# Kernel optimization log

Hardware: AMD Instinct MI355X
Metric: run time of the kernel (lower is better)

The kernel has to match this reference:

```python
import jax, jax.numpy as jnp
import numpy as np

B, T, DIM = 4, 1024, 1024
HEADS, DH = 16, 64
MEM, CMEM, RATIO = 1024, 256, 4
KV = CMEM + MEM + T  # 2304
TOTAL_MEM = MEM + CMEM  # 1280
NEG = -np.finfo(np.float32).max


def shift(x):
    # Faithful port of the pad/flatten/reshape relative-position shift trick.
    b, h, i, j = x.shape
    x = jnp.concatenate([x, jnp.zeros((b, h, i, i), x.dtype)], axis=-1)  # [b,h,i,i+j]
    l = i + j - 1
    x = x.reshape(b, h, i * (i + j))
    pad = (-x.shape[-1]) % l
    x = jnp.pad(x, ((0, 0), (0, 0), (0, pad)))
    x = x.reshape(b, h, -1, l)
    return x[:, :, :i, i - 1:]  # [b,h,i,j]


def setup_inputs() -> dict:
    key = jax.random.key(0)
    ks = jax.random.split(key, 10)
    s = 0.02
    return {
        "x": jax.random.normal(ks[0], (B, T, DIM), jnp.float32),
        "mem": jax.random.normal(ks[1], (B, MEM, DIM), jnp.float32),
        "cmem": jax.random.normal(ks[2], (B, CMEM, DIM), jnp.float32),
        "pos_emb": jax.random.normal(ks[3], (HEADS, KV, DH), jnp.float32),
        "input_mask": jnp.ones((B, T), bool),
        "Wq": jax.random.normal(ks[4], (DIM, DIM), jnp.float32) * s,
        "Wkv": jax.random.normal(ks[5], (2 * DIM, DIM), jnp.float32) * s,
        "Wout": jax.random.normal(ks[6], (DIM, DIM), jnp.float32) * s,
        "bout": jnp.zeros((DIM,), jnp.float32),
        "conv_w": jax.random.normal(ks[7], (DIM, DIM, RATIO), jnp.float32) * s,
        "conv_b": jnp.zeros((DIM,), jnp.float32),
    }


def reference(x, mem, cmem, pos_emb, input_mask, Wq, Wkv, Wout, bout, conv_w, conv_b):
    b, t, e = x.shape
    scale = DH ** -0.5

    q = x @ Wq.T                                             # [b,t,e]
    kv_input = jnp.concatenate([cmem, mem, x], axis=1)       # [b,kv,e]
    kv_len = kv_input.shape[1]
    kv = kv_input @ Wkv.T                                    # [b,kv,2e]
    k, v = jnp.split(kv, 2, axis=-1)

    def mh(z):
        return z.reshape(z.shape[0], z.shape[1], HEADS, DH).transpose(0, 2, 1, 3)

    qh, kh, vh = mh(q), mh(k), mh(v)                         # [b,h,*,dh]

    dots = jnp.einsum('bhid,bhjd->bhij', qh, kh) * scale     # [b,h,t,kv]

    pe = pos_emb[:, -kv_len:].astype(qh.dtype)               # [h,kv,dh]
    pos_dots = shift(jnp.einsum('bhid,hjd->bhij', qh, pe) * scale)
    dots = dots + pos_dots

    # input mask (padded True over mem+cmem positions)
    m = input_mask[:, None, :, None] & input_mask[:, None, None, :]  # [b,1,t,t]
    m = jnp.pad(m, ((0, 0), (0, 0), (0, 0), (TOTAL_MEM, 0)), constant_values=True)
    dots = jnp.where(m, dots, NEG)

    # causal mask shifted by total memory length
    causal = jnp.triu(jnp.ones((t, t + TOTAL_MEM), bool), k=1 + TOTAL_MEM)
    dots = jnp.where(causal[None, None], NEG, dots)

    attn = jax.nn.softmax(dots, axis=-1)
    out = jnp.einsum('bhij,bhjd->bhid', attn, vh)
    out = out.transpose(0, 2, 1, 3).reshape(b, t, e)
    logits = out @ Wout.T + bout

    # memory update (eval path, calc_memory=True)
    queue = jnp.concatenate([mem, x], axis=1)                # [b,mem+t,e]
    new_mem = queue[:, -MEM:]
    old_mem = jax.lax.stop_gradient(queue[:, :-MEM])         # [b,t,e], t % RATIO == 0
    comp = jax.lax.conv_general_dilated(
        old_mem.transpose(0, 2, 1), conv_w, (RATIO,), 'VALID',
        dimension_numbers=('NCH', 'OIH', 'NCH')) + conv_b[None, :, None]
    comp = comp.transpose(0, 2, 1)                           # [b,t//RATIO,e]
    new_cmem = jnp.concatenate([cmem, comp], axis=1)[:, -CMEM:]

    return logits, new_mem, new_cmem
```

## Files before the change

kernel.cpp:

```cpp
#include <hip/hip_runtime.h>
#include <hip/hip_bf16.h>
#include <hip/hip_fp16.h>
#include <cstdint>
#include <cstddef>
#include <cstring>

using bf16 = __hip_bfloat16;

constexpr int TS    = 1024;
constexpr int DIM   = 1024;
constexpr int MEMN  = 1024;
constexpr int CMEMN = 256;
constexpr int KVN   = 2304;
constexpr int TMEM  = 1280;

typedef __attribute__((ext_vector_type(8))) short short8;
typedef __attribute__((ext_vector_type(4))) float f32x4;

__device__ __forceinline__ unsigned short f2bf_us(float f){
    __hip_bfloat16 t = __float2bfloat16(f);
    unsigned short us; memcpy(&us, &t, 2); return us;
}
__device__ __forceinline__ int sw8(int row){ return (row & 7) ^ ((row >> 3) & 7); }

__device__ __forceinline__ short8 ldfrag(const unsigned short* base, int row, int chunk) {
    int ch = chunk ^ sw8(row);
    return *(const short8*)(base + row*64 + ch*8);
}
__device__ __forceinline__ void gl2lds16(const void* g, void* l) {
    __builtin_amdgcn_global_load_lds(
        (const __attribute__((address_space(1))) void*)g,
        (__attribute__((address_space(3))) void*)l, 16, 0, 0);
}

__global__ __launch_bounds__(256) void pack(
    const float* __restrict__ x, const float* __restrict__ memp,
    const float* __restrict__ cmem, const float* __restrict__ Wq,
    const float* __restrict__ Wkv, const float* __restrict__ Wout,
    const float* __restrict__ cw, const float* __restrict__ pe,
    unsigned short* __restrict__ kvin, unsigned short* __restrict__ wqb,
    unsigned short* __restrict__ wkvb, unsigned short* __restrict__ woutb,
    unsigned short* __restrict__ cw2b, unsigned short* __restrict__ peb)
{
    const size_t t8 = ((size_t)blockIdx.x * 256 + threadIdx.x) * 8;
    unsigned short h[8];
    if (t8 < 9437184) {
        size_t g = t8 >> 10;
        int cc = (int)(t8 & 1023);
        int b = (int)(g / KVN), j = (int)(g % KVN);
        const float* src;
        if (j < CMEMN)      src = cmem + ((size_t)b*CMEMN + j)*1024 + cc;
        else if (j < TMEM)  src = memp + ((size_t)b*MEMN + (j - CMEMN))*1024 + cc;
        else                src = x    + ((size_t)b*TS   + (j - TMEM))*1024 + cc;
        float4 f0 = *(const float4*)src; float4 f1 = *(const float4*)(src + 4);
        h[0]=f2bf_us(f0.x); h[1]=f2bf_us(f0.y); h[2]=f2bf_us(f0.z); h[3]=f2bf_us(f0.w);
        h[4]=f2bf_us(f1.x); h[5]=f2bf_us(f1.y); h[6]=f2bf_us(f1.z); h[7]=f2bf_us(f1.w);
        *(uint4*)(kvin + t8) = *(const uint4*)h;
    } else if (t8 < 13631488) {
        const float* src; unsigned short* dst; float sc = 1.0f;
        if (t8 < 10485760)      { src = Wq   + (t8 - 9437184);  dst = wqb   + (t8 - 9437184); sc = 0.125f; }
        else if (t8 < 12582912) { src = Wkv  + (t8 - 10485760); dst = wkvb  + (t8 - 10485760); }
        else                    { src = Wout + (t8 - 12582912); dst = woutb + (t8 - 12582912); }
        float4 f0 = *(const float4*)src; float4 f1 = *(const float4*)(src + 4);
        h[0]=f2bf_us(f0.x*sc); h[1]=f2bf_us(f0.y*sc); h[2]=f2bf_us(f0.z*sc); h[3]=f2bf_us(f0.w*sc);
        h[4]=f2bf_us(f1.x*sc); h[5]=f2bf_us(f1.y*sc); h[6]=f2bf_us(f1.z*sc); h[7]=f2bf_us(f1.w*sc);
        *(uint4*)dst = *(const uint4*)h;
    } else if (t8 < 17825792) {
        size_t o8 = t8 - 13631488;
        int o = (int)(o8 >> 12); int rem = (int)(o8 & 4095);
        int r = rem >> 10, i = rem & 1023;
        #pragma unroll
        for (int p = 0; p < 8; ++p) h[p] = f2bf_us(cw[(o << 12) + (i + p)*4 + r]);
        *(uint4*)(cw2b + o8) = *(const uint4*)h;
    } else {
        size_t o8 = t8 - 17825792;
        const float* src = pe + o8;
        float4 f0 = *(const float4*)src; float4 f1 = *(const float4*)(src + 4);
        h[0]=f2bf_us(f0.x); h[1]=f2bf_us(f0.y); h[2]=f2bf_us(f0.z); h[3]=f2bf_us(f0.w);
        h[4]=f2bf_us(f1.x); h[5]=f2bf_us(f1.y); h[6]=f2bf_us(f1.z); h[7]=f2bf_us(f1.w);
        *(uint4*)(peb + o8) = *(const uint4*)h;
    }
}

template<int EPI, int QMODE>
__global__ __launch_bounds__(256) void gemm_mfma(
    const bf16* __restrict__ Abf, const bf16* __restrict__ Bbf,
    const float* __restrict__ bias, void* __restrict__ Cptr,
    void* __restrict__ C2, int M, int N, int K)
{
    __shared__ alignas(16) unsigned short As[128*64];
    __shared__ alignas(16) unsigned short Bs[128*64];
    const int tid = threadIdx.x, lane = tid & 63, w = tid >> 6;
    const int quad = lane >> 4, colq = lane & 15;
    const int wm = w >> 1, wn = w & 1;
    const int m0 = blockIdx.x * 128, n0 = blockIdx.y * 128;
    size_t abase;
    if (QMODE == 0)      abase = (size_t)m0 * K;
    else if (QMODE == 1) abase = ((size_t)((m0 >> 10)*KVN + TMEM + (m0 & 1023))) * 1024;
    else                 abase = ((size_t)((m0 >> 8)*KVN + CMEMN)) * 1024 + (size_t)(m0 & 255) * 4096;
    const unsigned short* Ag = (const unsigned short*)Abf + abase;
    const unsigned short* Bg = (const unsigned short*)Bbf + (size_t)n0 * K;

    const int srow0 = w*32 + (lane >> 3);
    const int sch2  = lane & 7;

    f32x4 acc[4][4];
    #pragma unroll
    for (int i = 0; i < 4; ++i)
        #pragma unroll
        for (int j = 0; j < 4; ++j) acc[i][j] = (f32x4){0.f,0.f,0.f,0.f};

    for (int k0 = 0; k0 < K; k0 += 64) {
        __syncthreads();
        #pragma unroll
        for (int c = 0; c < 4; ++c) {
            int rr = srow0 + c*8;
            int ch = sch2 ^ sw8(rr);
            gl2lds16(Ag + (size_t)rr*K + k0 + ch*8, &As[(w*32 + c*8)*64]);
            gl2lds16(Bg + (size_t)rr*K + k0 + ch*8, &Bs[(w*32 + c*8)*64]);
        }
        __syncthreads();
        short8 af[4][2], bfr[4][2];
        #pragma unroll
        for (int i = 0; i < 4; ++i) {
            af[i][0]  = ldfrag(As, wm*64 + i*16 + colq, quad);
            af[i][1]  = ldfrag(As, wm*64 + i*16 + colq, 4 + quad);
            bfr[i][0] = ldfrag(Bs, wn*64 + i*16 + colq, quad);
            bfr[i][1] = ldfrag(Bs, wn*64 + i*16 + colq, 4 + quad);
        }
        #pragma unroll
        for (int i = 0; i < 4; ++i)
            #pragma unroll
            for (int j = 0; j < 4; ++j) {
                f32x4 t = __builtin_amdgcn_mfma_f32_16x16x32_bf16(af[i][0], bfr[j][0], acc[i][j], 0, 0, 0);
                acc[i][j] = __builtin_amdgcn_mfma_f32_16x16x32_bf16(af[i][1], bfr[j][1], t, 0, 0, 0);
            }
    }
    if (EPI == 2) {
        const int b = m0 / KVN;
        const int jj0 = (m0 - b*KVN) + wm*64;
        if (n0 < 1024) {
            bf16* kn = (bf16*)Cptr;
            #pragma unroll
            for (int j = 0; j < 4; ++j) {
                int col = n0 + wn*64 + j*16 + colq;
                #pragma unroll
                for (int i = 0; i < 4; ++i)
                    #pragma unroll
                    for (int r = 0; r < 4; ++r)
                        kn[(size_t)(b*KVN + jj0 + i*16 + quad*4 + r)*1024 + col] =
                            __float2bfloat16(acc[i][j][r]);
            }
        } else {
            unsigned short* vp = (unsigned short*)C2;
            #pragma unroll
            for (int j = 0; j < 4; ++j) {
                int col = n0 + wn*64 + j*16 + colq;
                int hh = (col >> 6) & 15, d = col & 63;
                #pragma unroll
                for (int i = 0; i < 4; ++i) {
                    int jjb = jj0 + i*16 + quad*4;
                    ushort4 u;
                    u.x = f2bf_us(acc[i][j][0]); u.y = f2bf_us(acc[i][j][1]);
                    u.z = f2bf_us(acc[i][j][2]); u.w = f2bf_us(acc[i][j][3]);
                    *(ushort4*)(vp + ((size_t)((b*16 + hh)*64 + d))*KVN + jjb) = u;
                }
            }
        }
    } else {
        #pragma unroll
        for (int j = 0; j < 4; ++j) {
            int col = n0 + wn*64 + j*16 + colq;
            float bj = bias ? bias[col] : 0.0f;
            #pragma unroll
            for (int i = 0; i < 4; ++i)
                #pragma unroll
                for (int r = 0; r < 4; ++r) {
                    size_t row = (size_t)(m0 + wm*64 + i*16 + quad*4 + r);
                    float v = acc[i][j][r] + bj;
                    if (EPI == 1) ((bf16*)Cptr)[row*N + col] = __float2bfloat16(v);
                    else          ((float*)Cptr)[row*N + col] = v;
                }
        }
    }
}

__global__ __launch_bounds__(256) void attn(
    const unsigned short* __restrict__ qg,
    const unsigned short* __restrict__ kq,
    const unsigned short* __restrict__ vh,
    const unsigned short* __restrict__ peb,
    bf16* __restrict__ out)
{
    __shared__ alignas(16) unsigned short Kt[64*64];
    __shared__ alignas(16) unsigned short Vt[64*64];
    __shared__ alignas(16) unsigned short PEr[256*64];
    __shared__ alignas(16) unsigned short Pb[128*64];

    const int tid  = threadIdx.x;
    const int lane = tid & 63, w = tid >> 6;
    const int quad = lane >> 4, colq = lane & 15;
    const int jr = lane >> 3, l7 = lane & 7;

    const int bx = blockIdx.x;
    const int b = bx & 3, h = (bx >> 2) & 15, q0 = (bx >> 6) * 128;

    #pragma unroll
    for (int c = 0; c < 4; ++c) {
        int row = c*32 + w*8 + jr;
        gl2lds16(qg + ((size_t)(b*1024 + q0 + row))*1024 + h*64 + (l7 ^ sw8(row))*8,
                 &Pb[(c*32 + w*8)*64]);
    }
    const int c0p = 896 - q0;
    #pragma unroll
    for (int c = 0; c < 4; ++c) {
        int cg = c0p + c*32 + w*8 + jr;
        int slot = cg & 255;
        gl2lds16(peb + ((size_t)h*KVN + cg)*64 + (l7 ^ sw8(slot))*8,
                 &PEr[((c0p + c*32 + w*8) & 255)*64]);
    }
    __syncthreads();
    short8 qa[2][2];
    #pragma unroll
    for (int it2 = 0; it2 < 2; ++it2) {
        qa[it2][0] = ldfrag(Pb, 32*w + 16*it2 + colq, quad);
        qa[it2][1] = ldfrag(Pb, 32*w + 16*it2 + colq, 4 + quad);
    }

    f32x4 oacc[2][4];
    float l_[2][4];
    #pragma unroll
    for (int it2 = 0; it2 < 2; ++it2) {
        #pragma unroll
        for (int dt = 0; dt < 4; ++dt) oacc[it2][dt] = (f32x4){0.f,0.f,0.f,0.f};
        #pragma unroll
        for (int r = 0; r < 4; ++r) l_[it2][r] = 0.f;
    }
    const f32x4 zero4 = (f32x4){0.f,0.f,0.f,0.f};
    const int nkv = min(36, ((q0 + 1407) >> 6) + 1);

    for (int kvt = 0; kvt < nkv; ++kvt) {
        const int kv0 = kvt * 64;
        __syncthreads();
        #pragma unroll
        for (int c = 0; c < 2; ++c) {
            int row = c*32 + w*8 + jr;
            gl2lds16(kq + ((size_t)(b*KVN + kv0 + row))*1024 + h*64 + (l7 ^ sw8(row))*8,
                     &Kt[(c*32 + w*8)*64]);
        }
        #pragma unroll
        for (int c = 0; c < 2; ++c) {
            int drow = c*32 + w*8 + jr;
            gl2lds16(vh + ((size_t)((b*16 + h)*64 + drow))*KVN + kv0 + (l7 ^ sw8(drow))*8,
                     &Vt[(c*32 + w*8)*64]);
        }
        const int cbase = kv0 - q0 + 1024;
        #pragma unroll
        for (int c = 0; c < 2; ++c) {
            int cg = cbase + c*32 + w*8 + jr;
            int cs = min(cg, KVN - 1);
            int slot = cg & 255;
            gl2lds16(peb + ((size_t)h*KVN + cs)*64 + (l7 ^ sw8(slot))*8,
                     &PEr[((cbase + c*32 + w*8) & 255)*64]);
        }
        __syncthreads();

        short8 kf[4][2], vf[4][2];
        #pragma unroll
        for (int nt = 0; nt < 4; ++nt) {
            kf[nt][0] = ldfrag(Kt, nt*16 + colq, quad);
            kf[nt][1] = ldfrag(Kt, nt*16 + colq, 4 + quad);
            vf[nt][0] = ldfrag(Vt, nt*16 + colq, quad);
            vf[nt][1] = ldfrag(Vt, nt*16 + colq, 4 + quad);
        }

        #pragma unroll
        for (int it2 = 0; it2 < 2; ++it2) {
            f32x4 facc[4];
            #pragma unroll
            for (int nt = 0; nt < 4; ++nt) {
                f32x4 t = __builtin_amdgcn_mfma_f32_16x16x32_bf16(qa[it2][0], kf[nt][0], zero4, 0, 0, 0);
                facc[nt] = __builtin_amdgcn_mfma_f32_16x16x32_bf16(qa[it2][1], kf[nt][1], t, 0, 0, 0);
            }
            const int cb = kv0 - q0 + 1008 - 32*w - 16*it2;
            f32x4 pacc[5];
            #pragma unroll
            for (int pnt = 0; pnt < 5; ++pnt) {
                int slot = (cb + pnt*16 + colq) & 255;
                short8 b0 = ldfrag(PEr, slot, quad);
                short8 b1 = ldfrag(PEr, slot, 4 + quad);
                f32x4 t = __builtin_amdgcn_mfma_f32_16x16x32_bf16(qa[it2][0], b0, zero4, 0, 0, 0);
                pacc[pnt] = __builtin_amdgcn_mfma_f32_16x16x32_bf16(qa[it2][1], b1, t, 0, 0, 0);
            }
            const int prow0 = 32*w + 16*it2 + 4*quad;
            #pragma unroll
            for (int r = 0; r < 4; ++r) {
                int tt = colq + 15 - 4*quad - r;
                int src = (lane & 48) | (tt & 15);
                float sh[5];
                #pragma unroll
                for (int p = 0; p < 5; ++p) sh[p] = __shfl(pacc[p][r], src, 64);
                int ig = q0 + prow0 + r;
                float lsum = 0.f;
                float ps[4];
                #pragma unroll
                for (int nt = 0; nt < 4; ++nt) {
                    float g = (tt < 16) ? sh[nt] : sh[nt + 1];
                    float v = facc[nt][r] + g;
                    int jg = kv0 + nt*16 + colq;
                    float s = (jg - ig > TMEM) ? -1e30f : v;
                    ps[nt] = __expf(s);
                    lsum += ps[nt];
                }
                l_[it2][r] += lsum;
                int prow = prow0 + r;
                int swp = sw8(prow);
                #pragma unroll
                for (int nt = 0; nt < 4; ++nt) {
                    int cc = nt*16 + colq;
                    Pb[prow*64 + (((cc >> 3) ^ swp))*8 + (cc & 7)] = f2bf_us(ps[nt]);
                }
            }
            short8 pa0 = ldfrag(Pb, 32*w + 16*it2 + colq, quad);
            short8 pa1 = ldfrag(Pb, 32*w + 16*it2 + colq, 4 + quad);
            #pragma unroll
            for (int dt = 0; dt < 4; ++dt) {
                f32x4 t = __builtin_amdgcn_mfma_f32_16x16x32_bf16(pa0, vf[dt][0], oacc[it2][dt], 0, 0, 0);
                oacc[it2][dt] = __builtin_amdgcn_mfma_f32_16x16x32_bf16(pa1, vf[dt][1], t, 0, 0, 0);
            }
        }
    }

    #pragma unroll
    for (int it2 = 0; it2 < 2; ++it2) {
        #pragma unroll
        for (int r = 0; r < 4; ++r) {
            float lt = l_[it2][r];
            #pragma unroll
            for (int off = 1; off < 16; off <<= 1) lt += __shfl_xor(lt, off, 64);
            float inv = 1.0f / lt;
            size_t row = (size_t)(b*1024 + q0 + 32*w + 16*it2 + 4*quad + r);
            #pragma unroll
            for (int dt = 0; dt < 4; ++dt)
                out[row*1024 + h*64 + dt*16 + colq] = __float2bfloat16(oacc[it2][dt][r] * inv);
        }
    }
}

__global__ __launch_bounds__(256) void copy_u4(const uint4* __restrict__ src,
                                               uint4* __restrict__ dst, int n)
{
    int i = blockIdx.x * 256 + threadIdx.x;
    if (i < n) dst[i] = src[i];
}

extern "C" void kernel_launch(void* const* d_in, const int* in_sizes, int n_in,
                              void* d_out, int out_size, void* d_ws, size_t ws_size,
                              hipStream_t stream)
{
    const float* x    = (const float*)d_in[0];
    const float* memp = (const float*)d_in[1];
    const float* cmem = (const float*)d_in[2];
    const float* pe   = (const float*)d_in[3];
    const float* Wq   = (const float*)d_in[5];
    const float* Wkv  = (const float*)d_in[6];
    const float* Wout = (const float*)d_in[7];
    const float* bout = (const float*)d_in[8];
    const float* cw   = (const float*)d_in[9];
    const float* cb   = (const float*)d_in[10];
    float* outp = (float*)d_out;

    char* wsb = (char*)d_ws;
    unsigned short* kvin  = (unsigned short*)(wsb);
    unsigned short* knat  = (unsigned short*)(wsb + 18874368);
    unsigned short* vhb   = (unsigned short*)(wsb + 37748736);
    unsigned short* qb    = (unsigned short*)(wsb + 56623104);
    bf16*           ao    = (bf16*)(wsb + 65011712);
    unsigned short* wqb   = (unsigned short*)(wsb + 73400320);
    unsigned short* wkvb  = (unsigned short*)(wsb + 75497472);
    unsigned short* woutb = (unsigned short*)(wsb + 79691776);
    unsigned short* cw2b  = (unsigned short*)(wsb + 81788928);
    unsigned short* peb   = (unsigned short*)(wsb + 90177536);

    pack<<<dim3(9856), 256, 0, stream>>>(x, memp, cmem, Wq, Wkv, Wout, cw, pe,
        kvin, wqb, wkvb, woutb, cw2b, peb);
    gemm_mfma<1,1><<<dim3(32, 8), 256, 0, stream>>>((const bf16*)kvin, (const bf16*)wqb,
        nullptr, qb, nullptr, 4096, 1024, 1024);
    gemm_mfma<2,0><<<dim3(72, 16), 256, 0, stream>>>((const bf16*)kvin, (const bf16*)wkvb,
        nullptr, knat, vhb, 9216, 2048, 1024);
    attn<<<dim3(512), 256, 0, stream>>>(qb, knat, vhb, peb, ao);
    gemm_mfma<0,0><<<dim3(32, 8), 256, 0, stream>>>(ao, (const bf16*)woutb,
        bout, outp, nullptr, 4096, 1024, 1024);
    copy_u4<<<dim3(4096), 256, 0, stream>>>((const uint4*)x,
        (uint4*)(outp + 4194304), 1048576);
    gemm_mfma<0,2><<<dim3(8, 8), 256, 0, stream>>>((const bf16*)kvin, (const bf16*)cw2b,
        cb, outp + 8388608, nullptr, 1024, 1024, 4096);
}
```

Baseline: 561.9 us.

## Load attention K/V/PE fragments directly from global memory, drop LDS staging

The attention kernel no longer stages K, V and positional-embedding tiles in shared memory with block-wide barriers. Each wave now loads its MFMA operand fragments straight from global memory, and each block covers 64 queries instead of 128, so the grid doubles to 1024 blocks with launch bounds set for three blocks per CU. This removes __syncthreads and the LDS footprint to raise occupancy. In exchange K/V tiles are re-read by each wave (four times per block) and by twice as many blocks, leaning on L1/L2 and adding global load latency to every iteration.

```diff
diff --git a/kernel.cpp b/kernel.cpp
--- a/kernel.cpp
+++ b/kernel.cpp
@@ -185,165 +185,126 @@
     }
 }
 
-__global__ __launch_bounds__(256) void attn(
+__global__ __launch_bounds__(256, 3) void attn(
     const unsigned short* __restrict__ qg,
     const unsigned short* __restrict__ kq,
     const unsigned short* __restrict__ vh,
     const unsigned short* __restrict__ peb,
     bf16* __restrict__ out)
 {
-    __shared__ alignas(16) unsigned short Kt[64*64];
-    __shared__ alignas(16) unsigned short Vt[64*64];
-    __shared__ alignas(16) unsigned short PEr[256*64];
-    __shared__ alignas(16) unsigned short Pb[128*64];
+    __shared__ alignas(16) unsigned short Pb[64*64];
 
     const int tid  = threadIdx.x;
     const int lane = tid & 63, w = tid >> 6;
     const int quad = lane >> 4, colq = lane & 15;
-    const int jr = lane >> 3, l7 = lane & 7;
 
     const int bx = blockIdx.x;
-    const int b = bx & 3, h = (bx >> 2) & 15, q0 = (bx >> 6) * 128;
-
+    const int b = bx & 3, h = (bx >> 2) & 15, q0 = (bx >> 6) * 64;
+    const int i0 = q0 + 16*w;
+
+    const unsigned short* qp = qg + ((size_t)(b*1024 + i0 + colq))*1024 + h*64;
+    const short8 qa0 = *(const short8*)(qp + quad*8);
+    const short8 qa1 = *(const short8*)(qp + 32 + quad*8);
+
+    const unsigned short* kbase = kq  + ((size_t)(b*KVN))*1024 + h*64;
+    const unsigned short* vbase = vh  + ((size_t)((b*16 + h)*64))*KVN;
+    const unsigned short* pbase = peb + (size_t)h*KVN*64;
+
+    f32x4 oacc[4];
+    float l_[4];
     #pragma unroll
-    for (int c = 0; c < 4; ++c) {
-        int row = c*32 + w*8 + jr;
-        gl2lds16(qg + ((size_t)(b*1024 + q0 + row))*1024 + h*64 + (l7 ^ sw8(row))*8,
-                 &Pb[(c*32 + w*8)*64]);
-    }
-    const int c0p = 896 - q0;
+    for (int dt = 0; dt < 4; ++dt) oacc[dt] = (f32x4){0.f,0.f,0.f,0.f};
     #pragma unroll
-    for (int c = 0; c < 4; ++c) {
-        int cg = c0p + c*32 + w*8 + jr;
-        int slot = cg & 255;
-        gl2lds16(peb + ((size_t)h*KVN + cg)*64 + (l7 ^ sw8(slot))*8,
-                 &PEr[((c0p + c*32 + w*8) & 255)*64]);
-    }
-    __syncthreads();
-    short8 qa[2][2];
-    #pragma unroll
-    for (int it2 = 0; it2 < 2; ++it2) {
-        qa[it2][0] = ldfrag(Pb, 32*w + 16*it2 + colq, quad);
-        qa[it2][1] = ldfrag(Pb, 32*w + 16*it2 + colq, 4 + quad);
-    }
-
-    f32x4 oacc[2][4];
-    float l_[2][4];
-    #pragma unroll
-    for (int it2 = 0; it2 < 2; ++it2) {
-        #pragma unroll
-        for (int dt = 0; dt < 4; ++dt) oacc[it2][dt] = (f32x4){0.f,0.f,0.f,0.f};
-        #pragma unroll
-        for (int r = 0; r < 4; ++r) l_[it2][r] = 0.f;
-    }
+    for (int r = 0; r < 4; ++r) l_[r] = 0.f;
     const f32x4 zero4 = (f32x4){0.f,0.f,0.f,0.f};
-    const int nkv = min(36, ((q0 + 1407) >> 6) + 1);
+
+    const int nkv = min(36, ((i0 + 15 + TMEM) >> 6) + 1);
 
     for (int kvt = 0; kvt < nkv; ++kvt) {
         const int kv0 = kvt * 64;
-        __syncthreads();
-        #pragma unroll
-        for (int c = 0; c < 2; ++c) {
-            int row = c*32 + w*8 + jr;
-            gl2lds16(kq + ((size_t)(b*KVN + kv0 + row))*1024 + h*64 + (l7 ^ sw8(row))*8,
-                     &Kt[(c*32 + w*8)*64]);
-        }
-        #pragma unroll
-        for (int c = 0; c < 2; ++c) {
-            int drow = c*32 + w*8 + jr;
-            gl2lds16(vh + ((size_t)((b*16 + h)*64 + drow))*KVN + kv0 + (l7 ^ sw8(drow))*8,
-                     &Vt[(c*32 + w*8)*64]);
-        }
-        const int cbase = kv0 - q0 + 1024;
-        #pragma unroll
-        for (int c = 0; c < 2; ++c) {
-            int cg = cbase + c*32 + w*8 + jr;
-            int cs = min(cg, KVN - 1);
-            int slot = cg & 255;
-            gl2lds16(peb + ((size_t)h*KVN + cs)*64 + (l7 ^ sw8(slot))*8,
-                     &PEr[((cbase + c*32 + w*8) & 255)*64]);
-        }
-        __syncthreads();
-
-        short8 kf[4][2], vf[4][2];
+        const int cb = kv0 - i0 + 1008;
+        short8 pf[5][2];
+        #pragma unroll
+        for (int pnt = 0; pnt < 5; ++pnt) {
+            int cs = min(cb + pnt*16 + colq, KVN - 1);
+            const unsigned short* pp = pbase + (size_t)cs*64;
+            pf[pnt][0] = *(const short8*)(pp + quad*8);
+            pf[pnt][1] = *(const short8*)(pp + 32 + quad*8);
+        }
+        short8 kf[4][2];
         #pragma unroll
         for (int nt = 0; nt < 4; ++nt) {
-            kf[nt][0] = ldfrag(Kt, nt*16 + colq, quad);
-            kf[nt][1] = ldfrag(Kt, nt*16 + colq, 4 + quad);
-            vf[nt][0] = ldfrag(Vt, nt*16 + colq, quad);
-            vf[nt][1] = ldfrag(Vt, nt*16 + colq, 4 + quad);
-        }
-
-        #pragma unroll
-        for (int it2 = 0; it2 < 2; ++it2) {
-            f32x4 facc[4];
+            const unsigned short* kp = kbase + (size_t)(kv0 + nt*16 + colq)*1024;
+            kf[nt][0] = *(const short8*)(kp + quad*8);
+            kf[nt][1] = *(const short8*)(kp + 32 + quad*8);
+        }
+        f32x4 facc[4];
+        #pragma unroll
+        for (int nt = 0; nt < 4; ++nt) {
+            f32x4 t = __builtin_amdgcn_mfma_f32_16x16x32_bf16(qa0, kf[nt][0], zero4, 0, 0, 0);
+            facc[nt] = __builtin_amdgcn_mfma_f32_16x16x32_bf16(qa1, kf[nt][1], t, 0, 0, 0);
+        }
+        f32x4 pacc[5];
+        #pragma unroll
+        for (int pnt = 0; pnt < 5; ++pnt) {
+            f32x4 t = __builtin_amdgcn_mfma_f32_16x16x32_bf16(qa0, pf[pnt][0], zero4, 0, 0, 0);
+            pacc[pnt] = __builtin_amdgcn_mfma_f32_16x16x32_bf16(qa1, pf[pnt][1], t, 0, 0, 0);
+        }
+        short8 vf[4][2];
+        #pragma unroll
+        for (int dt = 0; dt < 4; ++dt) {
+            const unsigned short* vp = vbase + (size_t)(dt*16 + colq)*KVN + kv0;
+            vf[dt][0] = *(const short8*)(vp + quad*8);
+            vf[dt][1] = *(const short8*)(vp + 32 + quad*8);
+        }
+        const int prow0 = 16*w + 4*quad;
+        #pragma unroll
+        for (int r = 0; r < 4; ++r) {
+            int tt = colq + 15 - 4*quad - r;
+            int src = (lane & 48) | (tt & 15);
+            float sh[5];
+            #pragma unroll
+            for (int p = 0; p < 5; ++p) sh[p] = __shfl(pacc[p][r], src, 64);
+            int ig = i0 + 4*quad + r;
+            float lsum = 0.f;
+            float ps[4];
             #pragma unroll
             for (int nt = 0; nt < 4; ++nt) {
-                f32x4 t = __builtin_amdgcn_mfma_f32_16x16x32_bf16(qa[it2][0], kf[nt][0], zero4, 0, 0, 0);
-                facc[nt] = __builtin_amdgcn_mfma_f32_16x16x32_bf16(qa[it2][1], kf[nt][1], t, 0, 0, 0);
-            }
-            const int cb = kv0 - q0 + 1008 - 32*w - 16*it2;
-            f32x4 pacc[5];
-            #pragma unroll
-            for (int pnt = 0; pnt < 5; ++pnt) {
-                int slot = (cb + pnt*16 + colq) & 255;
-                short8 b0 = ldfrag(PEr, slot, quad);
-                short8 b1 = ldfrag(PEr, slot, 4 + quad);
-                f32x4 t = __builtin_amdgcn_mfma_f32_16x16x32_bf16(qa[it2][0], b0, zero4, 0, 0, 0);
-                pacc[pnt] = __builtin_amdgcn_mfma_f32_16x16x32_bf16(qa[it2][1], b1, t, 0, 0, 0);
-            }
-            const int prow0 = 32*w + 16*it2 + 4*quad;
-            #pragma unroll
-            for (int r = 0; r < 4; ++r) {
-                int tt = colq + 15 - 4*quad - r;
-                int src = (lane & 48) | (tt & 15);
-                float sh[5];
-                #pragma unroll
-                for (int p = 0; p < 5; ++p) sh[p] = __shfl(pacc[p][r], src, 64);
-                int ig = q0 + prow0 + r;
-                float lsum = 0.f;
-                float ps[4];
-                #pragma unroll
-                for (int nt = 0; nt < 4; ++nt) {
-                    float g = (tt < 16) ? sh[nt] : sh[nt + 1];
-                    float v = facc[nt][r] + g;
-                    int jg = kv0 + nt*16 + colq;
-                    float s = (jg - ig > TMEM) ? -1e30f : v;
-                    ps[nt] = __expf(s);
-                    lsum += ps[nt];
-                }
-                l_[it2][r] += lsum;
-                int prow = prow0 + r;
-                int swp = sw8(prow);
-                #pragma unroll
-                for (int nt = 0; nt < 4; ++nt) {
-                    int cc = nt*16 + colq;
-                    Pb[prow*64 + (((cc >> 3) ^ swp))*8 + (cc & 7)] = f2bf_us(ps[nt]);
-                }
-            }
-            short8 pa0 = ldfrag(Pb, 32*w + 16*it2 + colq, quad);
-            short8 pa1 = ldfrag(Pb, 32*w + 16*it2 + colq, 4 + quad);
-            #pragma unroll
-            for (int dt = 0; dt < 4; ++dt) {
-                f32x4 t = __builtin_amdgcn_mfma_f32_16x16x32_bf16(pa0, vf[dt][0], oacc[it2][dt], 0, 0, 0);
-                oacc[it2][dt] = __builtin_amdgcn_mfma_f32_16x16x32_bf16(pa1, vf[dt][1], t, 0, 0, 0);
-            }
+                float g = (tt < 16) ? sh[nt] : sh[nt + 1];
+                float v = facc[nt][r] + g;
+                int jg = kv0 + nt*16 + colq;
+                float s = (jg - ig > TMEM) ? -1e30f : v;
+                ps[nt] = __expf(s);
+                lsum += ps[nt];
+            }
+            l_[r] += lsum;
+            int prow = prow0 + r;
+            int swp = sw8(prow);
+            #pragma unroll
+            for (int nt = 0; nt < 4; ++nt) {
+                int cc = nt*16 + colq;
+                Pb[prow*64 + (((cc >> 3) ^ swp))*8 + (cc & 7)] = f2bf_us(ps[nt]);
+            }
+        }
+        short8 pa0 = ldfrag(Pb, 16*w + colq, quad);
+        short8 pa1 = ldfrag(Pb, 16*w + colq, 4 + quad);
+        #pragma unroll
+        for (int dt = 0; dt < 4; ++dt) {
+            f32x4 t = __builtin_amdgcn_mfma_f32_16x16x32_bf16(pa0, vf[dt][0], oacc[dt], 0, 0, 0);
+            oacc[dt] = __builtin_amdgcn_mfma_f32_16x16x32_bf16(pa1, vf[dt][1], t, 0, 0, 0);
         }
     }
 
     #pragma unroll
-    for (int it2 = 0; it2 < 2; ++it2) {
-        #pragma unroll
-        for (int r = 0; r < 4; ++r) {
-            float lt = l_[it2][r];
-            #pragma unroll
-            for (int off = 1; off < 16; off <<= 1) lt += __shfl_xor(lt, off, 64);
-            float inv = 1.0f / lt;
-            size_t row = (size_t)(b*1024 + q0 + 32*w + 16*it2 + 4*quad + r);
-            #pragma unroll
-            for (int dt = 0; dt < 4; ++dt)
-                out[row*1024 + h*64 + dt*16 + colq] = __float2bfloat16(oacc[it2][dt][r] * inv);
-        }
+    for (int r = 0; r < 4; ++r) {
+        float lt = l_[r];
+        #pragma unroll
+        for (int off = 1; off < 16; off <<= 1) lt += __shfl_xor(lt, off, 64);
+        float inv = 1.0f / lt;
+        size_t row = (size_t)(b*1024 + i0 + 4*quad + r);
+        #pragma unroll
+        for (int dt = 0; dt < 4; ++dt)
+            out[row*1024 + h*64 + dt*16 + colq] = __float2bfloat16(oacc[dt][r] * inv);
     }
 }
 
@@ -388,7 +349,7 @@
         nullptr, qb, nullptr, 4096, 1024, 1024);
     gemm_mfma<2,0><<<dim3(72, 16), 256, 0, stream>>>((const bf16*)kvin, (const bf16*)wkvb,
         nullptr, knat, vhb, 9216, 2048, 1024);
-    attn<<<dim3(512), 256, 0, stream>>>(qb, knat, vhb, peb, ao);
+    attn<<<dim3(1024), 256, 0, stream>>>(qb, knat, vhb, peb, ao);
     gemm_mfma<0,0><<<dim3(32, 8), 256, 0, stream>>>(ao, (const bf16*)woutb,
         bout, outp, nullptr, 4096, 1024, 1024);
     copy_u4<<<dim3(4096), 256, 0, stream>>>((const uint4*)x,
```

Result: slower. 676.8 us (+20.5%).

## Register-prefetch next KV/PE tile in attention loop, add setprio and occupancy hint

Applied to the files above, without the earlier changes.

The attention kernel now loads the next K, V and positional-embedding tile from global memory into registers while computing the current tile, then writes them to LDS at the top of the next iteration. This replaces the direct global-to-LDS loads that were issued and waited on inside each iteration. The goal is to hide global latency behind the MFMA work. It also raises wave priority around the MFMA sections and adds a launch-bounds minimum of 2 blocks per CU, at the cost of more register pressure and possible spills.

```diff
diff --git a/kernel.cpp b/kernel.cpp
--- a/kernel.cpp
+++ b/kernel.cpp
@@ -32,6 +32,7 @@
         (const __attribute__((address_space(1))) void*)g,
         (__attribute__((address_space(3))) void*)l, 16, 0, 0);
 }
+__device__ __forceinline__ short8 ldg8(const unsigned short* p){ return *(const short8*)p; }
 
 __global__ __launch_bounds__(256) void pack(
     const float* __restrict__ x, const float* __restrict__ memp,
@@ -185,7 +186,7 @@
     }
 }
 
-__global__ __launch_bounds__(256) void attn(
+__global__ __launch_bounds__(256, 2) void attn(
     const unsigned short* __restrict__ qg,
     const unsigned short* __restrict__ kq,
     const unsigned short* __restrict__ vh,
@@ -227,6 +228,14 @@
         qa[it2][1] = ldfrag(Pb, 32*w + 16*it2 + colq, 4 + quad);
     }
 
+    const unsigned short* kbase = kq  + (size_t)b*KVN*1024 + h*64;
+    const unsigned short* vbase = vh  + ((size_t)((b*16 + h)*64))*KVN;
+    const unsigned short* pbase = peb + (size_t)h*KVN*64;
+
+    const int row0 = w*8 + jr, row1 = 32 + w*8 + jr;
+    const int ch0 = (l7 ^ sw8(row0))*8;
+    const int ch1 = (l7 ^ sw8(row1))*8;
+
     f32x4 oacc[2][4];
     float l_[2][4];
     #pragma unroll
@@ -239,31 +248,46 @@
     const f32x4 zero4 = (f32x4){0.f,0.f,0.f,0.f};
     const int nkv = min(36, ((q0 + 1407) >> 6) + 1);
 
+    short8 kr0, kr1, vr0, vr1, pr0, pr1;
+    {
+        kr0 = ldg8(kbase + (size_t)(row0)*1024 + ch0);
+        kr1 = ldg8(kbase + (size_t)(row1)*1024 + ch1);
+        vr0 = ldg8(vbase + (size_t)row0*KVN + ch0);
+        vr1 = ldg8(vbase + (size_t)row1*KVN + ch1);
+        int cb = 0 - q0 + 1024;
+        int cg0 = cb + row0, cg1 = cb + row1;
+        pr0 = ldg8(pbase + (size_t)min(cg0, KVN-1)*64 + ch0);
+        pr1 = ldg8(pbase + (size_t)min(cg1, KVN-1)*64 + ch1);
+    }
+
     for (int kvt = 0; kvt < nkv; ++kvt) {
         const int kv0 = kvt * 64;
-        __syncthreads();
-        #pragma unroll
-        for (int c = 0; c < 2; ++c) {
-            int row = c*32 + w*8 + jr;
-            gl2lds16(kq + ((size_t)(b*KVN + kv0 + row))*1024 + h*64 + (l7 ^ sw8(row))*8,
-                     &Kt[(c*32 + w*8)*64]);
-        }
-        #pragma unroll
-        for (int c = 0; c < 2; ++c) {
-            int drow = c*32 + w*8 + jr;
-            gl2lds16(vh + ((size_t)((b*16 + h)*64 + drow))*KVN + kv0 + (l7 ^ sw8(drow))*8,
-                     &Vt[(c*32 + w*8)*64]);
-        }
-        const int cbase = kv0 - q0 + 1024;
-        #pragma unroll
-        for (int c = 0; c < 2; ++c) {
-            int cg = cbase + c*32 + w*8 + jr;
-            int cs = min(cg, KVN - 1);
-            int slot = cg & 255;
-            gl2lds16(peb + ((size_t)h*KVN + cs)*64 + (l7 ^ sw8(slot))*8,
-                     &PEr[((cbase + c*32 + w*8) & 255)*64]);
-        }
-        __syncthreads();
+        asm volatile("s_waitcnt lgkmcnt(0)" ::: "memory");
+        __builtin_amdgcn_s_barrier();
+        *(short8*)(&Kt[row0*64 + l7*8]) = kr0;
+        *(short8*)(&Kt[row1*64 + l7*8]) = kr1;
+        *(short8*)(&Vt[row0*64 + l7*8]) = vr0;
+        *(short8*)(&Vt[row1*64 + l7*8]) = vr1;
+        {
+            int cb = kv0 - q0 + 1024;
+            int s0 = (cb + row0) & 255, s1 = (cb + row1) & 255;
+            *(short8*)(&PEr[s0*64 + l7*8]) = pr0;
+            *(short8*)(&PEr[s1*64 + l7*8]) = pr1;
+        }
+        if (kvt + 1 < nkv) {
+            int kvn = kv0 + 64;
+            kr0 = ldg8(kbase + (size_t)(kvn + row0)*1024 + ch0);
+            kr1 = ldg8(kbase + (size_t)(kvn + row1)*1024 + ch1);
+            vr0 = ldg8(vbase + (size_t)row0*KVN + kvn + ch0);
+            vr1 = ldg8(vbase + (size_t)row1*KVN + kvn + ch1);
+            int cb2 = kvn - q0 + 1024;
+            int cg0 = cb2 + row0, cg1 = cb2 + row1;
+            pr0 = ldg8(pbase + (size_t)min(cg0, KVN-1)*64 + ch0);
+            pr1 = ldg8(pbase + (size_t)min(cg1, KVN-1)*64 + ch1);
+        }
+        __builtin_amdgcn_sched_barrier(0);
+        asm volatile("s_waitcnt lgkmcnt(0)" ::: "memory");
+        __builtin_amdgcn_s_barrier();
 
         short8 kf[4][2], vf[4][2];
         #pragma unroll
@@ -277,6 +301,7 @@
         #pragma unroll
         for (int it2 = 0; it2 < 2; ++it2) {
             f32x4 facc[4];
+            __builtin_amdgcn_s_setprio(1);
             #pragma unroll
             for (int nt = 0; nt < 4; ++nt) {
                 f32x4 t = __builtin_amdgcn_mfma_f32_16x16x32_bf16(qa[it2][0], kf[nt][0], zero4, 0, 0, 0);
@@ -292,6 +317,7 @@
                 f32x4 t = __builtin_amdgcn_mfma_f32_16x16x32_bf16(qa[it2][0], b0, zero4, 0, 0, 0);
                 pacc[pnt] = __builtin_amdgcn_mfma_f32_16x16x32_bf16(qa[it2][1], b1, t, 0, 0, 0);
             }
+            __builtin_amdgcn_s_setprio(0);
             const int prow0 = 32*w + 16*it2 + 4*quad;
             #pragma unroll
             for (int r = 0; r < 4; ++r) {
@@ -323,11 +349,13 @@
             }
             short8 pa0 = ldfrag(Pb, 32*w + 16*it2 + colq, quad);
             short8 pa1 = ldfrag(Pb, 32*w + 16*it2 + colq, 4 + quad);
+            __builtin_amdgcn_s_setprio(1);
             #pragma unroll
             for (int dt = 0; dt < 4; ++dt) {
                 f32x4 t = __builtin_amdgcn_mfma_f32_16x16x32_bf16(pa0, vf[dt][0], oacc[it2][dt], 0, 0, 0);
                 oacc[it2][dt] = __builtin_amdgcn_mfma_f32_16x16x32_bf16(pa1, vf[dt][1], t, 0, 0, 0);
             }
+            __builtin_amdgcn_s_setprio(0);
         }
     }
 
```

After: 583.5 us. 3.9% more time.
